# Performance work log

Hardware: AMD Instinct MI355X
Metric: run time of the kernel (lower is better)

## Reference

```python
import jax, jax.numpy as jnp
import numpy as np

DIM = 512
EPS = 1e-8
LN_EPS = 1e-5


def _layernorm(x, g, b):
    mu = jnp.mean(x, axis=-1, keepdims=True)
    var = jnp.mean(jnp.square(x - mu), axis=-1, keepdims=True)
    return (x - mu) * jax.lax.rsqrt(var + LN_EPS) * g + b


def setup_inputs() -> dict:
    key = jax.random.key(0)
    ks = jax.random.split(key, 8)
    b, i, j, d = 8, 2048, 2048, DIM
    s = 1.0 / np.sqrt(d)
    return {
        "inputs": jax.random.normal(ks[0], (b, i, d), dtype=jnp.float32),
        "context": jax.random.normal(ks[1], (b, j, d), dtype=jnp.float32),
        "g_in": jnp.ones((d,), jnp.float32),
        "b_in": jnp.zeros((d,), jnp.float32),
        "g_ctx": jnp.ones((d,), jnp.float32),
        "b_ctx": jnp.zeros((d,), jnp.float32),
        "Wq": jax.random.uniform(ks[2], (d, d), jnp.float32, -s, s),
        "bq": jnp.zeros((d,), jnp.float32),
        "Wk": jax.random.uniform(ks[3], (d, d), jnp.float32, -s, s),
        "bk": jnp.zeros((d,), jnp.float32),
        "Wv": jax.random.uniform(ks[4], (d, d), jnp.float32, -s, s),
        "bv": jnp.zeros((d,), jnp.float32),
    }


def reference(inputs, context, g_in, b_in, g_ctx, b_ctx, Wq, bq, Wk, bk, Wv, bv):
    scale = DIM ** (-0.5)
    x = _layernorm(inputs, g_in, b_in)
    c = _layernorm(context, g_ctx, b_ctx)
    q = x @ Wq + bq          # [b,i,d]
    k = c @ Wk + bk          # [b,j,d]
    v = c @ Wv + bv          # [b,j,d]
    dots = jnp.einsum('bid,bjd->bij', q, k) * scale
    # NOTE: non-standard softmax over the QUERY axis (dim=1), then eps shift
    attn = jax.nn.softmax(dots, axis=1) + EPS
    # second renormalization over the KEY axis (dim=2)
    mean_attn = attn / (jnp.sum(attn, axis=2, keepdims=True) + EPS)
    updates = jnp.einsum('bjd,bij->bid', v, mean_attn)
    return updates
```

## Files before the change

kernel.cpp:

```cpp
#include <hip/hip_runtime.h>
#include <hip/hip_bf16.h>
#include <math.h>

#define EPSF 1e-8f
#define LN_EPSF 1e-5f
#define SCALE_QK 0.04419417382415922f

typedef unsigned short ushort_t;
typedef __bf16 bhalf;
typedef bhalf bhalf8 __attribute__((ext_vector_type(8)));
typedef float f32x4 __attribute__((ext_vector_type(4)));

__device__ __forceinline__ float b2f(ushort_t u) {
    return __uint_as_float((unsigned)u << 16);
}
__device__ __forceinline__ ushort_t f2b(float f) {
    unsigned x = __float_as_uint(f);
    return (ushort_t)((x + 0x7fffu + ((x >> 16) & 1u)) >> 16);
}
__device__ __forceinline__ unsigned pk2(float lo, float hi) {
    return (unsigned)f2b(lo) | ((unsigned)f2b(hi) << 16);
}
__device__ __forceinline__ void gload16(const ushort_t* g, ushort_t* l) {
    __builtin_amdgcn_global_load_lds(
        (const __attribute__((address_space(1))) unsigned int*)g,
        (__attribute__((address_space(3))) unsigned int*)l, 16, 0, 0);
}

__global__ __launch_bounds__(256) void mv_bias_kernel(
    const float* __restrict__ Wq, const float* __restrict__ Wk,
    const float* __restrict__ bq, const float* __restrict__ bk,
    float* __restrict__ wqbk, float* __restrict__ wkbq, float* __restrict__ cc)
{
    __shared__ float ls[4];
    const int y = blockIdx.y;
    const int t = threadIdx.x;
    if (y == 2) {
        if (blockIdx.x != 0) return;
        float s = bq[t] * bk[t] + bq[t + 256] * bk[t + 256];
#pragma unroll
        for (int off = 32; off > 0; off >>= 1) s += __shfl_down(s, off, 64);
        int lane = t & 63, w = t >> 6;
        if (lane == 0) ls[w] = s;
        __syncthreads();
        if (t == 0) cc[0] = ls[0] + ls[1] + ls[2] + ls[3];
        return;
    }
    const float* W = y ? Wk : Wq;
    const float* v = y ? bq : bk;
    float* o = y ? wkbq : wqbk;
    const int row = blockIdx.x * 16 + (t >> 4);
    const int l = t & 15;
    const float* wr = W + (size_t)row * 512 + l * 32;
    const float* vr = v + l * 32;
    float s = 0.f;
#pragma unroll
    for (int c = 0; c < 32; ++c) s += wr[c] * vr[c];
#pragma unroll
    for (int off = 8; off > 0; off >>= 1) s += __shfl_down(s, off, 16);
    if (l == 0) o[row] = s;
}

__global__ __launch_bounds__(256) void ln_apply_kernel(
    const float* __restrict__ X1, const float* __restrict__ X2,
    const float* __restrict__ g1, const float* __restrict__ b1,
    const float* __restrict__ g2, const float* __restrict__ b2,
    const float* __restrict__ wb1, const float* __restrict__ wb2,
    ushort_t* __restrict__ O1, ushort_t* __restrict__ O2,
    float* __restrict__ T1, float* __restrict__ T2)
{
    const bool sec = blockIdx.y != 0;
    const float* X = sec ? X2 : X1;
    const float* g = sec ? g2 : g1;
    const float* b = sec ? b2 : b1;
    const float* wb = sec ? wb2 : wb1;
    ushort_t* O = sec ? O2 : O1;
    float* T = sec ? T2 : T1;
    const size_t base = (size_t)blockIdx.x * 512;
    const int t = threadIdx.x;
    float2 x = ((const float2*)(X + base))[t];
    float s = x.x + x.y;
    float q = fmaf(x.x, x.x, x.y * x.y);
#pragma unroll
    for (int off = 32; off > 0; off >>= 1) {
        s += __shfl_down(s, off, 64);
        q += __shfl_down(q, off, 64);
    }
    __shared__ float ls[4], lq[4], mv[2], ld[4];
    int lane = t & 63, w = t >> 6;
    if (lane == 0) { ls[w] = s; lq[w] = q; }
    __syncthreads();
    if (t == 0) {
        float st = ls[0] + ls[1] + ls[2] + ls[3];
        float qt = lq[0] + lq[1] + lq[2] + lq[3];
        float mu = st * (1.0f / 512.0f);
        float var = qt * (1.0f / 512.0f) - mu * mu;
        mv[0] = mu;
        mv[1] = rsqrtf(var + LN_EPSF);
    }
    __syncthreads();
    const float mu = mv[0], rstd = mv[1];
    float2 gg = ((const float2*)g)[t];
    float2 bb = ((const float2*)b)[t];
    float2 ww = ((const float2*)wb)[t];
    float o0 = (x.x - mu) * rstd * gg.x + bb.x;
    float o1 = (x.y - mu) * rstd * gg.y + bb.y;
    ((unsigned*)O)[blockIdx.x * 256 + t] = pk2(o0, o1);
    float d = o0 * ww.x + o1 * ww.y;
#pragma unroll
    for (int off = 32; off > 0; off >>= 1) d += __shfl_down(d, off, 64);
    if (lane == 0) ld[w] = d;
    __syncthreads();
    if (t == 0) T[blockIdx.x] = ld[0] + ld[1] + ld[2] + ld[3];
}

__global__ __launch_bounds__(256) void wprep_kernel(
    const float* __restrict__ Wq, const float* __restrict__ Wk,
    const float* __restrict__ Wv,
    ushort_t* __restrict__ Wqb, ushort_t* __restrict__ Wkb,
    ushort_t* __restrict__ WvT)
{
    const int z = blockIdx.z;
    if (z < 2) {
        const float* W = z ? Wk : Wq;
        ushort_t* T = z ? Wkb : Wqb;
        size_t idx = ((size_t)(blockIdx.y * 16 + blockIdx.x)) * 1024 + threadIdx.x * 4;
        float4 f = *(const float4*)(W + idx);
        uint2 u;
        u.x = pk2(f.x, f.y);
        u.y = pk2(f.z, f.w);
        *(uint2*)(T + idx) = u;
        return;
    }
    __shared__ float tile[32][33];
    int tx = threadIdx.x & 31, ty = threadIdx.x >> 5;
    int r0 = blockIdx.y * 32, c0 = blockIdx.x * 32;
#pragma unroll
    for (int p = 0; p < 4; ++p)
        tile[ty + p * 8][tx] = Wv[(size_t)(r0 + ty + p * 8) * 512 + c0 + tx];
    __syncthreads();
#pragma unroll
    for (int p = 0; p < 4; ++p)
        WvT[(size_t)(c0 + ty + p * 8) * 512 + r0 + tx] = f2b(tile[tx][ty + p * 8]);
}

__global__ __launch_bounds__(256) void colrecip_kernel(
    const float* __restrict__ cs, float* __restrict__ cr,
    ushort_t* __restrict__ crs)
{
    int t = blockIdx.x * 256 + threadIdx.x;
    float r = 1.0f / cs[t];
    cr[t] = r;
    crs[t] = f2b(r);
}

template <int MODE>
__global__ __launch_bounds__(256) void mfma_gemm_kernel(
    const ushort_t* __restrict__ A, const ushort_t* __restrict__ B,
    void* __restrict__ Cout,
    const float* __restrict__ bias,
    const float* __restrict__ t1,
    const float* __restrict__ t2,
    const float* __restrict__ cc,
    float* __restrict__ colsum,
    const float* __restrict__ crcol,
    const ushort_t* __restrict__ crs,
    int K, int N, size_t strideA, size_t strideB, size_t strideC,
    float scale)
{
    __shared__ __align__(16) ushort_t As[128 * 64];
    __shared__ __align__(16) ushort_t Bs[128 * 64];
    __shared__ __align__(16) ushort_t crs_lds[(MODE == 2) ? 2048 : 8];
    const int tid = threadIdx.x;

    const int nbx = gridDim.x, nby = gridDim.y, nbz = gridDim.z;
    const int nwg = nbx * nby * nbz;
    int bx, by, bz;
    if ((nwg & 7) == 0) {
        int lin = blockIdx.x + nbx * (blockIdx.y + nby * blockIdx.z);
        int swz = (lin & 7) * (nwg >> 3) + (lin >> 3);
        const int sx = __builtin_ctz(nbx), sy = __builtin_ctz(nby);
        bx = swz & (nbx - 1);
        by = (swz >> sx) & (nby - 1);
        bz = swz >> (sx + sy);
    } else {
        bx = blockIdx.x; by = blockIdx.y; bz = blockIdx.z;
    }

    const ushort_t* Ab = A + strideA * bz;
    const ushort_t* Bb = B + strideB * bz;
    const int m0 = by * 128;
    const int n0 = bx * 128;
    const int wave = tid >> 6;
    const int lane = tid & 63;
    const int fm = lane & 15;
    const int fq = lane >> 4;
    const int fq4 = fq * 4;
    const int fm7 = fm & 7;
    const int wm = (wave >> 1) * 64;
    const int wn = (wave & 1) * 64;

    const int lrow = lane >> 3;
    const int lchunk = lane & 7;
    const int scs = lchunk ^ lrow;

    const ushort_t* aSrc[4]; const ushort_t* bSrc[4];
    ushort_t* aDst[4]; ushort_t* bDst[4];
#pragma unroll
    for (int p = 0; p < 4; ++p) {
        int row = wave * 32 + p * 8 + lrow;
        aSrc[p] = Ab + (size_t)(m0 + row) * K + scs * 8;
        bSrc[p] = Bb + (size_t)(n0 + row) * K + scs * 8;
        aDst[p] = As + (wave * 32 + p * 8) * 64 + lane * 8;
        bDst[p] = Bs + (wave * 32 + p * 8) * 64 + lane * 8;
    }

    if (MODE == 2) {
        uint4 c4 = *(const uint4*)(crs + (size_t)bz * 2048 + tid * 8);
        *(uint4*)&crs_lds[tid * 8] = c4;
    }

    const int cBase = fq ^ fm7;
    const ushort_t* aFrag[4]; const ushort_t* bFrag[4];
#pragma unroll
    for (int t = 0; t < 4; ++t) {
        aFrag[t] = As + (wm + t * 16 + fm) * 64;
        bFrag[t] = Bs + (wn + t * 16 + fm) * 64;
    }

    f32x4 acc[4][4];
    f32x4 sacc[4];
#pragma unroll
    for (int i = 0; i < 4; ++i) {
        sacc[i] = (f32x4){0.f, 0.f, 0.f, 0.f};
#pragma unroll
        for (int j = 0; j < 4; ++j) acc[i][j] = (f32x4){0.f, 0.f, 0.f, 0.f};
    }

    for (int k0 = 0; k0 < K; k0 += 64) {
        __syncthreads();
#pragma unroll
        for (int p = 0; p < 4; ++p) {
            gload16(aSrc[p] + k0, aDst[p]);
            gload16(bSrc[p] + k0, bDst[p]);
        }
        __syncthreads();
#pragma unroll
        for (int s = 0; s < 2; ++s) {
            const int off = ((cBase ^ (s << 2)) << 3);
            bhalf8 af[4], bfr[4];
#pragma unroll
            for (int u = 0; u < 4; ++u) {
                af[u]  = *(const bhalf8*)(aFrag[u] + off);
                bfr[u] = *(const bhalf8*)(bFrag[u] + off);
            }
#pragma unroll
            for (int i = 0; i < 4; ++i)
#pragma unroll
                for (int j = 0; j < 4; ++j)
                    acc[i][j] = __builtin_amdgcn_mfma_f32_16x16x32_bf16(
                        bfr[j], af[i], acc[i][j], 0, 0, 0);
            if (MODE == 2) {
                bhalf8 bc = *(const bhalf8*)&crs_lds[k0 + (s << 5) + (fq << 3)];
#pragma unroll
                for (int i = 0; i < 4; ++i)
                    sacc[i] = __builtin_amdgcn_mfma_f32_16x16x32_bf16(
                        bc, af[i], sacc[i], 0, 0, 0);
            }
        }
    }

    if (MODE == 2) {
        float* C = (float*)Cout + strideC * bz;
#pragma unroll
        for (int ti = 0; ti < 4; ++ti) {
            const int row = m0 + wm + ti * 16 + fm;
            const float rs = 1.0f / (sacc[ti][0] + 2.049e-5f);
            float* Cr = C + (size_t)row * N + n0 + wn + fq4;
#pragma unroll
            for (int tj = 0; tj < 4; ++tj) {
                f32x4 v;
#pragma unroll
                for (int r = 0; r < 4; ++r) v[r] = acc[ti][tj][r] * rs;
                *(f32x4*)(Cr + tj * 16) = v;
            }
        }
    } else if (MODE == 1) {
        ushort_t* C = (ushort_t*)Cout + strideC * bz;
        const float cv = cc[0];
        f32x4 t2c[4];
#pragma unroll
        for (int tj = 0; tj < 4; ++tj) {
            float4 tv = *(const float4*)(t2 + (size_t)bz * 2048 +
                                         n0 + wn + tj * 16 + fq4);
            t2c[tj][0] = tv.x + cv;
            t2c[tj][1] = tv.y + cv;
            t2c[tj][2] = tv.z + cv;
            t2c[tj][3] = tv.w + cv;
        }
        float psum[4][4];
#pragma unroll
        for (int tj = 0; tj < 4; ++tj)
#pragma unroll
            for (int r = 0; r < 4; ++r) psum[tj][r] = 0.f;
#pragma unroll
        for (int ti = 0; ti < 4; ++ti) {
            const int row = m0 + wm + ti * 16 + fm;
            const float t1v = t1[(size_t)bz * 2048 + row];
            ushort_t* Cr = C + (size_t)row * N + n0 + wn + fq4;
#pragma unroll
            for (int tj = 0; tj < 4; ++tj) {
                ushort_t h0 = f2b(__expf((acc[ti][tj][0] + t1v + t2c[tj][0]) * scale));
                ushort_t h1 = f2b(__expf((acc[ti][tj][1] + t1v + t2c[tj][1]) * scale));
                ushort_t h2 = f2b(__expf((acc[ti][tj][2] + t1v + t2c[tj][2]) * scale));
                ushort_t h3 = f2b(__expf((acc[ti][tj][3] + t1v + t2c[tj][3]) * scale));
                uint2 u;
                u.x = (unsigned)h0 | ((unsigned)h1 << 16);
                u.y = (unsigned)h2 | ((unsigned)h3 << 16);
                *(uint2*)(Cr + tj * 16) = u;
                psum[tj][0] += b2f(h0);
                psum[tj][1] += b2f(h1);
                psum[tj][2] += b2f(h2);
                psum[tj][3] += b2f(h3);
            }
        }
#pragma unroll
        for (int tj = 0; tj < 4; ++tj)
#pragma unroll
            for (int r = 0; r < 4; ++r) {
                float v = psum[tj][r];
                v += __shfl_xor(v, 1, 64);
                v += __shfl_xor(v, 2, 64);
                v += __shfl_xor(v, 4, 64);
                v += __shfl_xor(v, 8, 64);
                psum[tj][r] = v;
            }
        float* colpart = (float*)&As[0];
        __syncthreads();
        if (tid < 128) colpart[tid] = 0.f;
        __syncthreads();
        if (fm == 0) {
#pragma unroll
            for (int tj = 0; tj < 4; ++tj)
#pragma unroll
                for (int r = 0; r < 4; ++r)
                    atomicAdd(&colpart[wn + tj * 16 + fq4 + r], psum[tj][r]);
        }
        __syncthreads();
        if (tid < 128)
            atomicAdd(&colsum[(size_t)bz * 2048 + n0 + tid], colpart[tid]);
    } else if (MODE == 3) {
        ushort_t* C = (ushort_t*)Cout + strideC * bz;
        f32x4 crv[4];
#pragma unroll
        for (int tj = 0; tj < 4; ++tj) {
            float4 cq = *(const float4*)(crcol + (size_t)bz * 2048 +
                                         n0 + wn + tj * 16 + fq4);
            crv[tj][0] = cq.x; crv[tj][1] = cq.y;
            crv[tj][2] = cq.z; crv[tj][3] = cq.w;
        }
#pragma unroll
        for (int ti = 0; ti < 4; ++ti) {
            const int row = m0 + wm + ti * 16 + fm;
            const float bvv = bias[row];
            ushort_t* Cr = C + (size_t)row * N + n0 + wn + fq4;
#pragma unroll
            for (int tj = 0; tj < 4; ++tj) {
                uint2 u;
                u.x = pk2((acc[ti][tj][0] + bvv) * crv[tj][0],
                          (acc[ti][tj][1] + bvv) * crv[tj][1]);
                u.y = pk2((acc[ti][tj][2] + bvv) * crv[tj][2],
                          (acc[ti][tj][3] + bvv) * crv[tj][3]);
                *(uint2*)(Cr + tj * 16) = u;
            }
        }
    } else {
        ushort_t* C = (ushort_t*)Cout + strideC * bz;
#pragma unroll
        for (int ti = 0; ti < 4; ++ti) {
            const int row = m0 + wm + ti * 16 + fm;
            ushort_t* Cr = C + (size_t)row * N + n0 + wn + fq4;
#pragma unroll
            for (int tj = 0; tj < 4; ++tj) {
                uint2 u;
                u.x = pk2(acc[ti][tj][0], acc[ti][tj][1]);
                u.y = pk2(acc[ti][tj][2], acc[ti][tj][3]);
                *(uint2*)(Cr + tj * 16) = u;
            }
        }
    }
}

extern "C" void kernel_launch(void* const* d_in, const int* in_sizes, int n_in,
                              void* d_out, int out_size, void* d_ws, size_t ws_size,
                              hipStream_t stream)
{
    const float* inputs  = (const float*)d_in[0];
    const float* context = (const float*)d_in[1];
    const float* g_in    = (const float*)d_in[2];
    const float* b_in    = (const float*)d_in[3];
    const float* g_ctx   = (const float*)d_in[4];
    const float* b_ctx   = (const float*)d_in[5];
    const float* Wq      = (const float*)d_in[6];
    const float* bq      = (const float*)d_in[7];
    const float* Wk      = (const float*)d_in[8];
    const float* bk      = (const float*)d_in[9];
    const float* Wv      = (const float*)d_in[10];
    const float* bv      = (const float*)d_in[11];
    float* out = (float*)d_out;

    const size_t QKV  = 8ull * 2048 * 512;
    const size_t WSZ  = 512ull * 512;
    const size_t DOTS = 8ull * 2048 * 2048;

    ushort_t* xln   = (ushort_t*)d_ws;
    ushort_t* cln   = xln + QKV;
    ushort_t* Wqb   = cln + QKV;
    ushort_t* Wkb   = Wqb + WSZ;
    ushort_t* WvT   = Wkb + WSZ;
    ushort_t* Mb    = WvT + WSZ;
    ushort_t* KM    = Mb + WSZ;
    ushort_t* vTs   = KM + QKV;
    ushort_t* edots = vTs + QKV;
    ushort_t* crs   = edots + DOTS;
    float* fbase    = (float*)(crs + 16384);
    float* colsum   = fbase;
    float* colrecip = colsum + 16384;
    float* t1       = colrecip + 16384;
    float* t2       = t1 + 16384;
    float* wqbk     = t2 + 16384;
    float* wkbq     = wqbk + 512;
    float* cc       = wkbq + 512;
    size_t need_bytes = (4 * QKV + 4 * WSZ + DOTS + 16384) * 2
                      + (4 * 16384 + 1024 + 1) * 4;
    if (ws_size < need_bytes) return;

    hipMemsetAsync(colsum, 0, 16384 * sizeof(float), stream);

    mv_bias_kernel<<<dim3(32, 3), 256, 0, stream>>>(Wq, Wk, bq, bk, wqbk, wkbq, cc);

    ln_apply_kernel<<<dim3(16384, 2), 256, 0, stream>>>(
        inputs, context, g_in, b_in, g_ctx, b_ctx, wqbk, wkbq, xln, cln, t1, t2);

    wprep_kernel<<<dim3(16, 16, 3), 256, 0, stream>>>(Wq, Wk, Wv, Wqb, Wkb, WvT);

    mfma_gemm_kernel<0><<<dim3(4, 4, 1), 256, 0, stream>>>(
        Wqb, Wkb, Mb, nullptr, nullptr, nullptr, nullptr, nullptr, nullptr, nullptr,
        512, 512, 0, 0, 0, 1.f);

    mfma_gemm_kernel<0><<<dim3(4, 128, 1), 256, 0, stream>>>(
        cln, Mb, KM, nullptr, nullptr, nullptr, nullptr, nullptr, nullptr, nullptr,
        512, 512, 0, 0, 0, 1.f);

    mfma_gemm_kernel<1><<<dim3(16, 16, 8), 256, 0, stream>>>(
        xln, KM, edots, nullptr, t1, t2, cc, colsum, nullptr, nullptr,
        512, 2048, (size_t)2048 * 512, (size_t)2048 * 512, (size_t)2048 * 2048,
        SCALE_QK);

    colrecip_kernel<<<64, 256, 0, stream>>>(colsum, colrecip, crs);

    mfma_gemm_kernel<3><<<dim3(16, 4, 8), 256, 0, stream>>>(
        WvT, cln, vTs, bv, nullptr, nullptr, nullptr, nullptr, colrecip, nullptr,
        512, 2048, 0, (size_t)2048 * 512, (size_t)512 * 2048, 1.f);

    mfma_gemm_kernel<2><<<dim3(4, 16, 8), 256, 0, stream>>>(
        edots, vTs, out, nullptr, nullptr, nullptr, nullptr, nullptr, nullptr, crs,
        2048, 512, (size_t)2048 * 2048, (size_t)512 * 2048, (size_t)2048 * 512,
        1.f);
}
```

Before: 315.2 us.

## Replace QK^T exp GEMM with 256x256-tile double-buffered 512-thread kernel

Moves the dots GEMM with fused exp and column-sum epilogue into a dedicated kernel. The new kernel uses 256x256 output tiles, 8 waves of 128x64 sub-tiles, and double-buffered LDS with explicit vmcnt waits, so the next K-slice loads overlap compute. The larger tiles raise arithmetic intensity and halve the global atomics per column, while the prefetch hides load latency. In exchange it uses about 128KB of LDS and 128 accumulator registers per thread, which lowers occupancy, and it launches only 512 workgroups. The now-unused MODE 1 path and its parameters are dropped from the generic GEMM.

Result: faster. 303.4 us (-3.8%).

```diff
diff --git a/kernel.cpp b/kernel.cpp
--- a/kernel.cpp
+++ b/kernel.cpp
@@ -154,19 +154,196 @@
     crs[t] = f2b(r);
 }
 
+__global__ __launch_bounds__(512) void gemm256_exp_kernel(
+    const ushort_t* __restrict__ A, const ushort_t* __restrict__ B,
+    ushort_t* __restrict__ Cout,
+    const float* __restrict__ t1, const float* __restrict__ t2,
+    const float* __restrict__ cc, float* __restrict__ colsum,
+    int K, int N, size_t strideA, size_t strideB, size_t strideC,
+    float scale)
+{
+    __shared__ __align__(16) ushort_t As0[256 * 64];
+    __shared__ __align__(16) ushort_t As1[256 * 64];
+    __shared__ __align__(16) ushort_t Bs0[256 * 64];
+    __shared__ __align__(16) ushort_t Bs1[256 * 64];
+    const int tid = threadIdx.x;
+
+    const int nbx = gridDim.x, nby = gridDim.y;
+    const int nwg = nbx * nby * gridDim.z;
+    int lin = blockIdx.x + nbx * (blockIdx.y + nby * blockIdx.z);
+    int swz = (lin & 7) * (nwg >> 3) + (lin >> 3);
+    const int sx = __builtin_ctz(nbx), sy = __builtin_ctz(nby);
+    const int bx = swz & (nbx - 1);
+    const int by = (swz >> sx) & (nby - 1);
+    const int bz = swz >> (sx + sy);
+
+    const ushort_t* Ab = A + strideA * bz;
+    const ushort_t* Bb = B + strideB * bz;
+    const int m0 = by * 256;
+    const int n0 = bx * 256;
+    const int wave = tid >> 6;
+    const int lane = tid & 63;
+    const int fm = lane & 15;
+    const int fq = lane >> 4;
+    const int fq4 = fq * 4;
+    const int wm = (wave >> 2) * 128;
+    const int wn = (wave & 3) * 64;
+
+    const int lrow = lane >> 3;
+    const int lchunk = lane & 7;
+    const int scs = lchunk ^ lrow;
+
+    const ushort_t* aSrc[4]; const ushort_t* bSrc[4];
+#pragma unroll
+    for (int p = 0; p < 4; ++p) {
+        int row = wave * 32 + p * 8 + lrow;
+        aSrc[p] = Ab + (size_t)(m0 + row) * K + scs * 8;
+        bSrc[p] = Bb + (size_t)(n0 + row) * K + scs * 8;
+    }
+    const int dOff = wave * 2048 + lane * 8;
+
+    const int cBase = fq ^ (fm & 7);
+
+    f32x4 acc[8][4];
+#pragma unroll
+    for (int i = 0; i < 8; ++i)
+#pragma unroll
+        for (int j = 0; j < 4; ++j) acc[i][j] = (f32x4){0.f, 0.f, 0.f, 0.f};
+
+    auto stage = [&](ushort_t* Ad, ushort_t* Bd, int k0) {
+#pragma unroll
+        for (int p = 0; p < 4; ++p) {
+            gload16(aSrc[p] + k0, Ad + dOff + p * 512);
+            gload16(bSrc[p] + k0, Bd + dOff + p * 512);
+        }
+    };
+    auto compute = [&](const ushort_t* Asb, const ushort_t* Bsb) {
+#pragma unroll
+        for (int s = 0; s < 2; ++s) {
+            const int off = ((cBase ^ (s << 2)) << 3);
+            bhalf8 af[8], bfr[4];
+#pragma unroll
+            for (int u = 0; u < 8; ++u)
+                af[u] = *(const bhalf8*)(Asb + (wm + u * 16 + fm) * 64 + off);
+#pragma unroll
+            for (int u = 0; u < 4; ++u)
+                bfr[u] = *(const bhalf8*)(Bsb + (wn + u * 16 + fm) * 64 + off);
+#pragma unroll
+            for (int i = 0; i < 8; ++i)
+#pragma unroll
+                for (int j = 0; j < 4; ++j)
+                    acc[i][j] = __builtin_amdgcn_mfma_f32_16x16x32_bf16(
+                        bfr[j], af[i], acc[i][j], 0, 0, 0);
+        }
+    };
+
+#define WAITV8  { asm volatile("s_waitcnt vmcnt(8)" ::: "memory"); \
+                  __builtin_amdgcn_sched_barrier(0); }
+#define WAITV0  { asm volatile("s_waitcnt vmcnt(0)" ::: "memory"); \
+                  __builtin_amdgcn_sched_barrier(0); }
+#define FENCE_LGKM { asm volatile("s_waitcnt lgkmcnt(0)" ::: "memory"); \
+                     __builtin_amdgcn_sched_barrier(0); }
+
+    const int nk = K >> 6;
+    stage(As0, Bs0, 0);
+    stage(As1, Bs1, 64);
+    for (int t = 0; t < nk - 2; t += 2) {
+        WAITV8;
+        __builtin_amdgcn_s_barrier();
+        compute(As0, Bs0);
+        FENCE_LGKM;
+        __builtin_amdgcn_s_barrier();
+        stage(As0, Bs0, (t + 2) << 6);
+        WAITV8;
+        __builtin_amdgcn_s_barrier();
+        compute(As1, Bs1);
+        FENCE_LGKM;
+        __builtin_amdgcn_s_barrier();
+        stage(As1, Bs1, (t + 3) << 6);
+    }
+    WAITV8;
+    __builtin_amdgcn_s_barrier();
+    compute(As0, Bs0);
+    WAITV0;
+    __builtin_amdgcn_s_barrier();
+    compute(As1, Bs1);
+#undef WAITV8
+#undef WAITV0
+#undef FENCE_LGKM
+
+    ushort_t* C = Cout + strideC * bz;
+    const float cv = cc[0];
+    f32x4 t2c[4];
+#pragma unroll
+    for (int nj = 0; nj < 4; ++nj) {
+        float4 tv = *(const float4*)(t2 + (size_t)bz * 2048 +
+                                     n0 + wn + nj * 16 + fq4);
+        t2c[nj][0] = tv.x + cv;
+        t2c[nj][1] = tv.y + cv;
+        t2c[nj][2] = tv.z + cv;
+        t2c[nj][3] = tv.w + cv;
+    }
+    float psum[4][4];
+#pragma unroll
+    for (int nj = 0; nj < 4; ++nj)
+#pragma unroll
+        for (int r = 0; r < 4; ++r) psum[nj][r] = 0.f;
+#pragma unroll
+    for (int mi = 0; mi < 8; ++mi) {
+        const int row = m0 + wm + mi * 16 + fm;
+        const float t1v = t1[(size_t)bz * 2048 + row];
+        ushort_t* Cr = C + (size_t)row * N + n0 + wn + fq4;
+#pragma unroll
+        for (int nj = 0; nj < 4; ++nj) {
+            ushort_t h0 = f2b(__expf((acc[mi][nj][0] + t1v + t2c[nj][0]) * scale));
+            ushort_t h1 = f2b(__expf((acc[mi][nj][1] + t1v + t2c[nj][1]) * scale));
+            ushort_t h2 = f2b(__expf((acc[mi][nj][2] + t1v + t2c[nj][2]) * scale));
+            ushort_t h3 = f2b(__expf((acc[mi][nj][3] + t1v + t2c[nj][3]) * scale));
+            uint2 u;
+            u.x = (unsigned)h0 | ((unsigned)h1 << 16);
+            u.y = (unsigned)h2 | ((unsigned)h3 << 16);
+            *(uint2*)(Cr + nj * 16) = u;
+            psum[nj][0] += b2f(h0);
+            psum[nj][1] += b2f(h1);
+            psum[nj][2] += b2f(h2);
+            psum[nj][3] += b2f(h3);
+        }
+    }
+#pragma unroll
+    for (int nj = 0; nj < 4; ++nj)
+#pragma unroll
+        for (int r = 0; r < 4; ++r) {
+            float v = psum[nj][r];
+            v += __shfl_xor(v, 1, 64);
+            v += __shfl_xor(v, 2, 64);
+            v += __shfl_xor(v, 4, 64);
+            v += __shfl_xor(v, 8, 64);
+            psum[nj][r] = v;
+        }
+    float* colpart = (float*)&As0[0];
+    __syncthreads();
+    if (tid < 256) colpart[tid] = 0.f;
+    __syncthreads();
+    if (fm == 0) {
+#pragma unroll
+        for (int nj = 0; nj < 4; ++nj)
+#pragma unroll
+            for (int r = 0; r < 4; ++r)
+                atomicAdd(&colpart[wn + nj * 16 + fq4 + r], psum[nj][r]);
+    }
+    __syncthreads();
+    if (tid < 256)
+        atomicAdd(&colsum[(size_t)bz * 2048 + n0 + tid], colpart[tid]);
+}
+
 template <int MODE>
 __global__ __launch_bounds__(256) void mfma_gemm_kernel(
     const ushort_t* __restrict__ A, const ushort_t* __restrict__ B,
     void* __restrict__ Cout,
     const float* __restrict__ bias,
-    const float* __restrict__ t1,
-    const float* __restrict__ t2,
-    const float* __restrict__ cc,
-    float* __restrict__ colsum,
     const float* __restrict__ crcol,
     const ushort_t* __restrict__ crs,
-    int K, int N, size_t strideA, size_t strideB, size_t strideC,
-    float scale)
+    int K, int N, size_t strideA, size_t strideB, size_t strideC)
 {
     __shared__ __align__(16) ushort_t As[128 * 64];
     __shared__ __align__(16) ushort_t Bs[128 * 64];
@@ -285,70 +462,6 @@
                 *(f32x4*)(Cr + tj * 16) = v;
             }
         }
-    } else if (MODE == 1) {
-        ushort_t* C = (ushort_t*)Cout + strideC * bz;
-        const float cv = cc[0];
-        f32x4 t2c[4];
-#pragma unroll
-        for (int tj = 0; tj < 4; ++tj) {
-            float4 tv = *(const float4*)(t2 + (size_t)bz * 2048 +
-                                         n0 + wn + tj * 16 + fq4);
-            t2c[tj][0] = tv.x + cv;
-            t2c[tj][1] = tv.y + cv;
-            t2c[tj][2] = tv.z + cv;
-            t2c[tj][3] = tv.w + cv;
-        }
-        float psum[4][4];
-#pragma unroll
-        for (int tj = 0; tj < 4; ++tj)
-#pragma unroll
-            for (int r = 0; r < 4; ++r) psum[tj][r] = 0.f;
-#pragma unroll
-        for (int ti = 0; ti < 4; ++ti) {
-            const int row = m0 + wm + ti * 16 + fm;
-            const float t1v = t1[(size_t)bz * 2048 + row];
-            ushort_t* Cr = C + (size_t)row * N + n0 + wn + fq4;
-#pragma unroll
-            for (int tj = 0; tj < 4; ++tj) {
-                ushort_t h0 = f2b(__expf((acc[ti][tj][0] + t1v + t2c[tj][0]) * scale));
-                ushort_t h1 = f2b(__expf((acc[ti][tj][1] + t1v + t2c[tj][1]) * scale));
-                ushort_t h2 = f2b(__expf((acc[ti][tj][2] + t1v + t2c[tj][2]) * scale));
-                ushort_t h3 = f2b(__expf((acc[ti][tj][3] + t1v + t2c[tj][3]) * scale));
-                uint2 u;
-                u.x = (unsigned)h0 | ((unsigned)h1 << 16);
-                u.y = (unsigned)h2 | ((unsigned)h3 << 16);
-                *(uint2*)(Cr + tj * 16) = u;
-                psum[tj][0] += b2f(h0);
-                psum[tj][1] += b2f(h1);
-                psum[tj][2] += b2f(h2);
-                psum[tj][3] += b2f(h3);
-            }
-        }
-#pragma unroll
-        for (int tj = 0; tj < 4; ++tj)
-#pragma unroll
-            for (int r = 0; r < 4; ++r) {
-                float v = psum[tj][r];
-                v += __shfl_xor(v, 1, 64);
-                v += __shfl_xor(v, 2, 64);
-                v += __shfl_xor(v, 4, 64);
-                v += __shfl_xor(v, 8, 64);
-                psum[tj][r] = v;
-            }
-        float* colpart = (float*)&As[0];
-        __syncthreads();
-        if (tid < 128) colpart[tid] = 0.f;
-        __syncthreads();
-        if (fm == 0) {
-#pragma unroll
-            for (int tj = 0; tj < 4; ++tj)
-#pragma unroll
-                for (int r = 0; r < 4; ++r)
-                    atomicAdd(&colpart[wn + tj * 16 + fq4 + r], psum[tj][r]);
-        }
-        __syncthreads();
-        if (tid < 128)
-            atomicAdd(&colsum[(size_t)bz * 2048 + n0 + tid], colpart[tid]);
     } else if (MODE == 3) {
         ushort_t* C = (ushort_t*)Cout + strideC * bz;
         f32x4 crv[4];
@@ -445,26 +558,25 @@
     wprep_kernel<<<dim3(16, 16, 3), 256, 0, stream>>>(Wq, Wk, Wv, Wqb, Wkb, WvT);
 
     mfma_gemm_kernel<0><<<dim3(4, 4, 1), 256, 0, stream>>>(
-        Wqb, Wkb, Mb, nullptr, nullptr, nullptr, nullptr, nullptr, nullptr, nullptr,
-        512, 512, 0, 0, 0, 1.f);
+        Wqb, Wkb, Mb, nullptr, nullptr, nullptr,
+        512, 512, 0, 0, 0);
 
     mfma_gemm_kernel<0><<<dim3(4, 128, 1), 256, 0, stream>>>(
-        cln, Mb, KM, nullptr, nullptr, nullptr, nullptr, nullptr, nullptr, nullptr,
-        512, 512, 0, 0, 0, 1.f);
-
-    mfma_gemm_kernel<1><<<dim3(16, 16, 8), 256, 0, stream>>>(
-        xln, KM, edots, nullptr, t1, t2, cc, colsum, nullptr, nullptr,
+        cln, Mb, KM, nullptr, nullptr, nullptr,
+        512, 512, 0, 0, 0);
+
+    gemm256_exp_kernel<<<dim3(8, 8, 8), 512, 0, stream>>>(
+        xln, KM, edots, t1, t2, cc, colsum,
         512, 2048, (size_t)2048 * 512, (size_t)2048 * 512, (size_t)2048 * 2048,
         SCALE_QK);
 
     colrecip_kernel<<<64, 256, 0, stream>>>(colsum, colrecip, crs);
 
     mfma_gemm_kernel<3><<<dim3(16, 4, 8), 256, 0, stream>>>(
-        WvT, cln, vTs, bv, nullptr, nullptr, nullptr, nullptr, colrecip, nullptr,
-        512, 2048, 0, (size_t)2048 * 512, (size_t)512 * 2048, 1.f);
+        WvT, cln, vTs, bv, colrecip, nullptr,
+        512, 2048, 0, (size_t)2048 * 512, (size_t)512 * 2048);
 
     mfma_gemm_kernel<2><<<dim3(4, 16, 8), 256, 0, stream>>>(
-        edots, vTs, out, nullptr, nullptr, nullptr, nullptr, nullptr, nullptr, crs,
-        2048, 512, (size_t)2048 * 2048, (size_t)512 * 2048, (size_t)2048 * 512,
-        1.f);
-}
+        edots, vTs, out, nullptr, nullptr, crs,
+        2048, 512, (size_t)2048 * 2048, (size_t)512 * 2048, (size_t)2048 * 512);
+}
```
